# Optimization experiments

Hardware: AMD Instinct MI355X
Metric: run time of the kernel (lower is better)

## Reference

```python
import jax, jax.numpy as jnp
import numpy as np

EMBED_DIM = 1024
NUM_HEADS = 16
DEPTH = 12
HEAD_DIM = EMBED_DIM // NUM_HEADS // 2  # 32
LAMBDA_INIT = float(0.8 - 0.6 * np.exp(-0.3 * DEPTH))
B, T = 2, 2048


def setup_inputs() -> dict:
    key = jax.random.key(0)
    ks = jax.random.split(key, 10)
    s = 0.02
    return {
        "query": jax.random.normal(ks[0], (B, T, EMBED_DIM), jnp.float32),
        "Wq": jax.random.normal(ks[1], (EMBED_DIM, EMBED_DIM), jnp.float32) * s,
        "Wk": jax.random.normal(ks[2], (EMBED_DIM, EMBED_DIM), jnp.float32) * s,
        "Wv": jax.random.normal(ks[3], (EMBED_DIM, EMBED_DIM), jnp.float32) * s,
        "Wo": jax.random.normal(ks[4], (EMBED_DIM, EMBED_DIM), jnp.float32) * s,
        "lambda_q1": jax.random.normal(ks[5], (HEAD_DIM,), jnp.float32) * 0.1,
        "lambda_k1": jax.random.normal(ks[6], (HEAD_DIM,), jnp.float32) * 0.1,
        "lambda_q2": jax.random.normal(ks[7], (HEAD_DIM,), jnp.float32) * 0.1,
        "lambda_k2": jax.random.normal(ks[8], (HEAD_DIM,), jnp.float32) * 0.1,
        "subln_w": jnp.ones((2 * HEAD_DIM,), jnp.float32),
    }


def reference(query, Wq, Wk, Wv, Wo, lambda_q1, lambda_k1, lambda_q2, lambda_k2, subln_w):
    Bsz, Tt, E = query.shape
    H, hd = NUM_HEADS, HEAD_DIM
    scaling = hd ** -0.5
    # projections (torch Linear: x @ W.T), W stored [out, in]
    q = jnp.einsum('bte,fe->btf', query, Wq).reshape(Bsz, Tt, 2 * H, hd).transpose(0, 2, 1, 3)
    k = jnp.einsum('bse,fe->bsf', query, Wk).reshape(Bsz, Tt, 2 * H, hd).transpose(0, 2, 1, 3)
    v = jnp.einsum('bse,fe->bsf', query, Wv).reshape(Bsz, Tt, H, 2 * hd).transpose(0, 2, 1, 3)
    q = q * scaling
    # dual attention map [B, 2H, T, T], softmax in fp32
    scores = jnp.einsum('bhtd,bhsd->bhts', q, k)
    attn_w = jax.nn.softmax(scores.astype(jnp.float32), axis=-1).astype(q.dtype)
    # learned lambda
    lam1 = jnp.exp(jnp.sum(lambda_q1 * lambda_k1))
    lam2 = jnp.exp(jnp.sum(lambda_q2 * lambda_k2))
    lam = lam1 - lam2 + LAMBDA_INIT
    aw = attn_w.reshape(Bsz, H, 2, Tt, Tt)
    aw = aw[:, :, 0] - lam * aw[:, :, 1]  # [B, H, T, T]
    attn = jnp.einsum('bhts,bhsd->bhtd', aw, v)  # [B, H, T, 2*hd]
    # RMSNorm over last dim (fp32), eps=1e-5, elementwise affine
    x32 = attn.astype(jnp.float32)
    normed = (x32 * jax.lax.rsqrt(jnp.mean(x32 * x32, axis=-1, keepdims=True) + 1e-5)).astype(attn.dtype)
    attn = normed * subln_w
    attn = attn * (1.0 - LAMBDA_INIT)
    out = attn.transpose(0, 2, 1, 3).reshape(Bsz, Tt, H * 2 * hd)
    return jnp.einsum('bte,fe->btf', out, Wo)
```

## Files before the change

### kernel.cpp

```cpp
#include <hip/hip_runtime.h>

typedef short bf16x8 __attribute__((ext_vector_type(8)));
typedef float f32x4 __attribute__((ext_vector_type(4)));
typedef float f32x16 __attribute__((ext_vector_type(16)));
typedef unsigned short ushort_t;
typedef unsigned int uint32;

#define LAMBDA_INIT 0.7836057665316245f
#define TT 2048
#define EE 1024

__device__ __forceinline__ ushort_t f2bf(float x) {
  uint32 b = __float_as_uint(x);
  b += 0x7fffu + ((b >> 16) & 1u);
  return (ushort_t)(b >> 16);
}

__device__ __forceinline__ uint32 cvtpk(float lo, float hi) {
  uint32 r;
  asm("v_cvt_pk_bf16_f32 %0, %1, %2" : "=v"(r) : "v"(lo), "v"(hi));
  return r;
}

__device__ __forceinline__ float fexp2(float x) {
#if __has_builtin(__builtin_amdgcn_exp2f)
  return __builtin_amdgcn_exp2f(x);
#else
  return exp2f(x);
#endif
}

__device__ __forceinline__ bf16x8 mkfrag(uint32 a, uint32 b, uint32 c, uint32 d) {
  union { uint32 w[4]; bf16x8 v; } u;
  u.w[0] = a; u.w[1] = b; u.w[2] = c; u.w[3] = d;
  return u.v;
}

__device__ __forceinline__ void gload16(const void* g, void* l) {
  __builtin_amdgcn_global_load_lds(
      (const __attribute__((address_space(1))) uint32*)g,
      (__attribute__((address_space(3))) uint32*)l, 16, 0, 0);
}

__global__ __launch_bounds__(256) void cvt_all(const float* __restrict__ X,
                                               const float* __restrict__ Wq,
                                               const float* __restrict__ Wk,
                                               const float* __restrict__ Wv,
                                               const float* __restrict__ Wo,
                                               ushort_t* __restrict__ out) {
  const int i = blockIdx.x * 256 + threadIdx.x;
  const float* src;
  int off;
  if (i < 1048576)      { src = X;  off = 0; }
  else if (i < 1310720) { src = Wq; off = 1048576; }
  else if (i < 1572864) { src = Wk; off = 1310720; }
  else if (i < 1835008) { src = Wv; off = 1572864; }
  else                  { src = Wo; off = 1835008; }
  const float4 v = reinterpret_cast<const float4*>(src)[i - off];
  ushort4 o;
  o.x = f2bf(v.x); o.y = f2bf(v.y); o.z = f2bf(v.z); o.w = f2bf(v.w);
  reinterpret_cast<ushort4*>(out)[i] = o;
}

__global__ __launch_bounds__(256) void gemm_bt(const ushort_t* __restrict__ A,
                                               const ushort_t* __restrict__ B,
                                               float* __restrict__ C,
                                               int M, int N, int K, float scale) {
  __shared__ ushort_t As[128 * 32];
  __shared__ ushort_t Bs[128 * 32];
  const int tid = threadIdx.x;
  const int lane = tid & 63, wid = tid >> 6;
  const int wr = wid >> 1, wc = wid & 1;
  const int r16 = lane & 15, g = lane >> 4;
  const int m0 = blockIdx.x * 128, n0 = blockIdx.y * 128;
  f32x4 acc[4][4] = {};
  for (int k0 = 0; k0 < K; k0 += 32) {
#pragma unroll
    for (int c = 0; c < 2; ++c) {
      int eo = wid * 1024 + c * 512 + lane * 8;
      int row = eo >> 5, col = eo & 31;
      gload16(A + (size_t)(m0 + row) * K + k0 + col, As + wid * 1024 + c * 512);
      gload16(B + (size_t)(n0 + row) * K + k0 + col, Bs + wid * 1024 + c * 512);
    }
    __syncthreads();
    bf16x8 af[4], bfg[4];
#pragma unroll
    for (int m = 0; m < 4; ++m)
      af[m] = *reinterpret_cast<const bf16x8*>(As + (wr * 64 + m * 16 + r16) * 32 + g * 8);
#pragma unroll
    for (int n = 0; n < 4; ++n)
      bfg[n] = *reinterpret_cast<const bf16x8*>(Bs + (wc * 64 + n * 16 + r16) * 32 + g * 8);
#pragma unroll
    for (int m = 0; m < 4; ++m)
#pragma unroll
      for (int n = 0; n < 4; ++n)
        acc[m][n] = __builtin_amdgcn_mfma_f32_16x16x32_bf16(af[m], bfg[n], acc[m][n], 0, 0, 0);
    __syncthreads();
  }
#pragma unroll
  for (int m = 0; m < 4; ++m)
#pragma unroll
    for (int n = 0; n < 4; ++n)
#pragma unroll
      for (int r = 0; r < 4; ++r) {
        int row = m0 + wr * 64 + m * 16 + g * 4 + r;
        int col = n0 + wc * 64 + n * 16 + r16;
        C[(size_t)row * N + col] = acc[m][n][r] * scale;
      }
}

#define SHALF(Sbase, Gbase)                                                  \
  do {                                                                       \
    _Pragma("unroll") for (int j_ = 0; j_ < 2; ++j_) {                       \
      const int c_ = wid * 2 + j_;                                           \
      gload16((Gbase) + (size_t)(c_ * 8 + (lane >> 3)) * EE +                \
                  (((lane & 7) ^ (lane >> 3)) << 3),                         \
              (Sbase) + c_ * 512);                                           \
    }                                                                        \
  } while (0)

#define CHUNK(mp)                                                            \
  do {                                                                       \
    __builtin_amdgcn_s_setprio(1);                                           \
    _Pragma("unroll") for (int mm_ = 0; mm_ < 2; ++mm_) {                    \
      const int m_ = (mp) * 2 + mm_;                                         \
      _Pragma("unroll") for (int n_ = 0; n_ < 4; ++n_) {                     \
        acc[m_][n_] = __builtin_amdgcn_mfma_f32_16x16x32_bf16(               \
            af[m_][0], bfr[n_][0], acc[m_][n_], 0, 0, 0);                    \
        acc[m_][n_] = __builtin_amdgcn_mfma_f32_16x16x32_bf16(               \
            af[m_][1], bfr[n_][1], acc[m_][n_], 0, 0, 0);                    \
      }                                                                      \
    }                                                                        \
    __builtin_amdgcn_s_setprio(0);                                           \
  } while (0)

__global__ __launch_bounds__(512, 2) void qkv_gemm256(const ushort_t* __restrict__ A,
                                                      const ushort_t* __restrict__ B,
                                                      ushort_t* __restrict__ C,
                                                      float scale) {
  __shared__ ushort_t Asm[2][16384];
  __shared__ ushort_t Bsm[2][16384];
  const int NKT = EE / 64;
  const int tid = threadIdx.x, lane = tid & 63, wid = tid >> 6;
  const int wr = wid >> 2, wc = wid & 3;
  const int r16 = lane & 15, g = lane >> 4;
  const int w = (blockIdx.x & 7) * 24 + (blockIdx.x >> 3);
  const int bx = w & 15, by = w >> 4;
  const int m0 = bx * 256, n0 = by * 256;
  const ushort_t* Ab = A + (size_t)m0 * EE;
  const ushort_t* Bb = B + (size_t)n0 * EE;

#pragma unroll
  for (int kt = 0; kt < 2; ++kt) {
    SHALF(Asm[kt], Ab + kt * 64);
    SHALF(Asm[kt] + 8192, Ab + (size_t)128 * EE + kt * 64);
    SHALF(Bsm[kt], Bb + kt * 64);
    SHALF(Bsm[kt] + 8192, Bb + (size_t)128 * EE + kt * 64);
  }

  f32x4 acc[8][4] = {};
  for (int t = 0; t < NKT; ++t) {
    const int b = t & 1;
    if (t < NKT - 1) asm volatile("s_waitcnt vmcnt(8)" ::: "memory");
    else             asm volatile("s_waitcnt vmcnt(0)" ::: "memory");
    __builtin_amdgcn_s_barrier();
    asm volatile("" ::: "memory");
    bf16x8 af[8][2], bfr[4][2];
#pragma unroll
    for (int m = 0; m < 8; ++m) {
      const int row = wr * 128 + m * 16 + r16;
#pragma unroll
      for (int kk = 0; kk < 2; ++kk)
        af[m][kk] = *reinterpret_cast<const bf16x8*>(
            Asm[b] + row * 64 + (((kk * 4 + g) ^ (r16 & 7)) << 3));
    }
#pragma unroll
    for (int n = 0; n < 4; ++n) {
      const int row = wc * 64 + n * 16 + r16;
#pragma unroll
      for (int kk = 0; kk < 2; ++kk)
        bfr[n][kk] = *reinterpret_cast<const bf16x8*>(
            Bsm[b] + row * 64 + (((kk * 4 + g) ^ (r16 & 7)) << 3));
    }
    asm volatile("s_waitcnt lgkmcnt(0)" ::: "memory");
    __builtin_amdgcn_s_barrier();
    asm volatile("" ::: "memory");
    const int ts = t + 2;
    const bool st = ts < NKT;
    if (st) SHALF(Asm[b], Ab + ts * 64);
    CHUNK(0);
    if (st) SHALF(Asm[b] + 8192, Ab + (size_t)128 * EE + ts * 64);
    CHUNK(1);
    if (st) SHALF(Bsm[b], Bb + ts * 64);
    CHUNK(2);
    if (st) SHALF(Bsm[b] + 8192, Bb + (size_t)128 * EE + ts * 64);
    CHUNK(3);
  }

  const size_t MN = (size_t)4096 * EE;
#pragma unroll
  for (int m = 0; m < 8; ++m)
#pragma unroll
    for (int n = 0; n < 4; ++n) {
      const int col = n0 + wc * 64 + n * 16 + r16;
      const int seg = col >> 10;
      const int cl = col & 1023;
      if (seg == 2) {
        int row0 = m0 + wr * 128 + m * 16 + g * 4;
        int bb2 = row0 >> 11, t0v = row0 & (TT - 1);
        ushort4 pk;
        pk.x = f2bf(acc[m][n][0]); pk.y = f2bf(acc[m][n][1]);
        pk.z = f2bf(acc[m][n][2]); pk.w = f2bf(acc[m][n][3]);
        *reinterpret_cast<ushort4*>(
            C + 2 * MN + ((size_t)(bb2 * 16 + (cl >> 6)) * 64 + (cl & 63)) * TT + t0v) = pk;
      } else {
        const float sc = (seg == 0) ? scale : 1.0f;
        const size_t base = (size_t)seg * MN;
#pragma unroll
        for (int r = 0; r < 4; ++r) {
          int row = m0 + wr * 128 + m * 16 + g * 4 + r;
          C[base + (size_t)row * EE + cl] = f2bf(acc[m][n][r] * sc);
        }
      }
    }
}


#define PHALF(sv, lacc, oT0, oT1, vf)                                                   \
  do {                                                                                  \
    float p_[16];                                                                       \
    _Pragma("unroll") for (int i_ = 0; i_ < 16; ++i_) p_[i_] = fexp2(sv[i_]);           \
    lacc += (((p_[0] + p_[1]) + (p_[2] + p_[3])) + ((p_[4] + p_[5]) + (p_[6] + p_[7]))) \
          + (((p_[8] + p_[9]) + (p_[10] + p_[11])) +                                    \
             ((p_[12] + p_[13]) + (p_[14] + p_[15])));                                  \
    auto wA_ = __builtin_amdgcn_permlane32_swap((int)cvtpk(p_[0], p_[1]),               \
                                                (int)cvtpk(p_[4], p_[5]), false, false);\
    auto wB_ = __builtin_amdgcn_permlane32_swap((int)cvtpk(p_[2], p_[3]),               \
                                                (int)cvtpk(p_[6], p_[7]), false, false);\
    auto wC_ = __builtin_amdgcn_permlane32_swap((int)cvtpk(p_[8], p_[9]),               \
                                                (int)cvtpk(p_[12], p_[13]), false, false);\
    auto wD_ = __builtin_amdgcn_permlane32_swap((int)cvtpk(p_[10], p_[11]),             \
                                                (int)cvtpk(p_[14], p_[15]), false, false);\
    bf16x8 pa0_ = mkfrag(wA_[0], wB_[0], wA_[1], wB_[1]);                               \
    bf16x8 pa1_ = mkfrag(wC_[0], wD_[0], wC_[1], wD_[1]);                               \
    oT0 = __builtin_amdgcn_mfma_f32_32x32x16_bf16(pa0_, vf[0][0], oT0, 0, 0, 0);        \
    oT0 = __builtin_amdgcn_mfma_f32_32x32x16_bf16(pa1_, vf[1][0], oT0, 0, 0, 0);        \
    oT1 = __builtin_amdgcn_mfma_f32_32x32x16_bf16(pa0_, vf[0][1], oT1, 0, 0, 0);        \
    oT1 = __builtin_amdgcn_mfma_f32_32x32x16_bf16(pa1_, vf[1][1], oT1, 0, 0, 0);        \
  } while (0)

#define STAGE3(Kdst, Vdst, kv0)                                                         \
  do {                                                                                  \
    const int r8_ = lane >> 3;                                                          \
    const int g_ = (lane & 7) ^ r8_;                                                    \
    _Pragma("unroll") for (int c2_ = 0; c2_ < 2; ++c2_) {                               \
      const int c_ = wid * 2 + c2_;                                                     \
      gload16(Kg + (size_t)((kv0) + c_ * 8 + r8_) * EE + g_ * 8,                        \
              (Kdst) + c_ * 512);                                                       \
      gload16(Vg + (size_t)(c_ * 8 + r8_) * TT + (kv0) + g_ * 8,                        \
              (Vdst) + c_ * 512);                                                       \
    }                                                                                   \
  } while (0)

__global__ __launch_bounds__(256, 2) void attn_fused(
    const ushort_t* __restrict__ Q, const ushort_t* __restrict__ K,
    const ushort_t* __restrict__ Vt,
    const float* __restrict__ lq1, const float* __restrict__ lk1,
    const float* __restrict__ lq2, const float* __restrict__ lk2,
    const float* __restrict__ w, ushort_t* __restrict__ X2) {
  __shared__ ushort_t Ksm[3][64 * 64];
  __shared__ ushort_t Vsm[3][64 * 64];
  const int tid = threadIdx.x, lane = tid & 63, wid = tid >> 6;
  const int l31 = lane & 31, hh = lane >> 5;
  const int bid = blockIdx.x;
  const int slice = (bid & 7) + 8 * (bid >> 7);
  const int qb = (bid >> 3) & 15;
  const int bb = slice >> 4, h = slice & 15;
  const int q0 = qb * 128 + wid * 32;

  float prod = (lane < 32) ? lq1[l31] * lk1[l31] : lq2[l31] * lk2[l31];
#pragma unroll
  for (int off = 1; off < 32; off <<= 1) prod += __shfl_xor(prod, off, 32);
  const float lam = __expf(__shfl(prod, 0, 64)) - __expf(__shfl(prod, 32, 64)) + LAMBDA_INIT;

  const ushort_t* Qp = Q + (size_t)(bb * TT + q0 + l31) * EE + h * 64 + hh * 8;
  const bf16x8 qf00 = *reinterpret_cast<const bf16x8*>(Qp);
  const bf16x8 qf01 = *reinterpret_cast<const bf16x8*>(Qp + 16);
  const bf16x8 qf10 = *reinterpret_cast<const bf16x8*>(Qp + 32);
  const bf16x8 qf11 = *reinterpret_cast<const bf16x8*>(Qp + 48);

  const ushort_t* Kg = K + (size_t)bb * TT * EE + h * 64;
  const ushort_t* Vg = Vt + (size_t)(bb * 16 + h) * 64 * TT;
  const int swz = (l31 & 7) << 3;

  f32x16 o00 = {}, o01 = {}, o10 = {}, o11 = {};
  float l0 = 0.f, l1 = 0.f;

  STAGE3(Ksm[0], Vsm[0], 0);
  STAGE3(Ksm[1], Vsm[1], 64);
  for (int it = 0; it < 32; ++it) {
    const ushort_t* Kt_ = Ksm[it % 3];
    const ushort_t* Vt_ = Vsm[it % 3];
    if (it < 31) asm volatile("s_waitcnt vmcnt(4)" ::: "memory");
    else         asm volatile("s_waitcnt vmcnt(0)" ::: "memory");
    __builtin_amdgcn_s_barrier();
    asm volatile("" ::: "memory");
    if (it + 2 < 32) {
      const int nb = (it + 2) % 3;
      STAGE3(Ksm[nb], Vsm[nb], (it + 2) * 64);
    }
#pragma unroll
    for (int s = 0; s < 2; ++s) {
      bf16x8 kf[2][2], vf[2][2];
#pragma unroll
      for (int hf = 0; hf < 2; ++hf)
#pragma unroll
        for (int ks = 0; ks < 2; ++ks)
          kf[hf][ks] = *reinterpret_cast<const bf16x8*>(
              Kt_ + (s * 32 + l31) * 64 + ((hf * 32 + ks * 16 + hh * 8) ^ swz));
#pragma unroll
      for (int ks = 0; ks < 2; ++ks)
#pragma unroll
        for (int dc = 0; dc < 2; ++dc)
          vf[ks][dc] = *reinterpret_cast<const bf16x8*>(
              Vt_ + (dc * 32 + l31) * 64 + ((s * 32 + ks * 16 + hh * 8) ^ swz));

      __builtin_amdgcn_s_setprio(1);
      const f32x16 zz = {};
      f32x16 s0_ = __builtin_amdgcn_mfma_f32_32x32x16_bf16(kf[0][0], qf00, zz, 0, 0, 0);
      s0_ = __builtin_amdgcn_mfma_f32_32x32x16_bf16(kf[0][1], qf01, s0_, 0, 0, 0);
      f32x16 s1_ = __builtin_amdgcn_mfma_f32_32x32x16_bf16(kf[1][0], qf10, zz, 0, 0, 0);
      s1_ = __builtin_amdgcn_mfma_f32_32x32x16_bf16(kf[1][1], qf11, s1_, 0, 0, 0);
      __builtin_amdgcn_s_setprio(0);
      PHALF(s0_, l0, o00, o01, vf);
      PHALF(s1_, l1, o10, o11, vf);
    }
  }

  {
    auto t0 = __builtin_amdgcn_permlane32_swap(__float_as_int(l0), __float_as_int(l0),
                                               false, false);
    l0 = __int_as_float(t0[0]) + __int_as_float(t0[1]);
    auto t1 = __builtin_amdgcn_permlane32_swap(__float_as_int(l1), __float_as_int(l1),
                                               false, false);
    l1 = __int_as_float(t1[0]) + __int_as_float(t1[1]);
  }

  const float w0v = w[l31];
  const float w1v = w[32 + l31];
#pragma unroll
  for (int r = 0; r < 16; ++r) {
    const int qrel = (r & 3) + 8 * (r >> 2) + 4 * hh;
    const float il0 = 1.0f / __shfl(l0, qrel, 64);
    const float il1 = lam / __shfl(l1, qrel, 64);
    const float x0 = o00[r] * il0 - o10[r] * il1;
    const float x1 = o01[r] * il0 - o11[r] * il1;
    float ss = x0 * x0 + x1 * x1;
#pragma unroll
    for (int off = 1; off < 32; off <<= 1) ss += __shfl_xor(ss, off, 64);
    const float sc = rsqrtf(ss * (1.0f / 64.0f) + 1e-5f) * (1.0f - LAMBDA_INIT);
    const size_t ob = (size_t)(bb * TT + q0 + qrel) * EE + h * 64 + l31;
    X2[ob] = f2bf(x0 * sc * w0v);
    X2[ob + 32] = f2bf(x1 * sc * w1v);
  }
}

extern "C" void kernel_launch(void* const* d_in, const int* in_sizes, int n_in,
                              void* d_out, int out_size, void* d_ws, size_t ws_size,
                              hipStream_t stream) {
  const float* X = (const float*)d_in[0];
  const float* Wq = (const float*)d_in[1];
  const float* Wk = (const float*)d_in[2];
  const float* Wv = (const float*)d_in[3];
  const float* Wo = (const float*)d_in[4];
  const float* lq1 = (const float*)d_in[5];
  const float* lk1 = (const float*)d_in[6];
  const float* lq2 = (const float*)d_in[7];
  const float* lk2 = (const float*)d_in[8];
  const float* slw = (const float*)d_in[9];

  const int M = 4096, E = EE;

  ushort_t* Xb = (ushort_t*)d_ws;
  ushort_t* Wqb = Xb + (size_t)M * E;
  ushort_t* Wob = Wqb + (size_t)3 * E * E;
  ushort_t* Qb = Wob + (size_t)E * E;
  ushort_t* Kb = Qb + (size_t)M * E;
  ushort_t* Vtb = Kb + (size_t)M * E;
  ushort_t* X2 = Vtb + (size_t)M * E;

  cvt_all<<<8192, 256, 0, stream>>>(X, Wq, Wk, Wv, Wo, Xb);

  qkv_gemm256<<<192, 512, 0, stream>>>(Xb, Wqb, Qb,
                                       0.17677669529663687f * 1.4426950408889634f);

  attn_fused<<<512, 256, 0, stream>>>(Qb, Kb, Vtb, lq1, lk1, lq2, lk2, slw, X2);

  gemm_bt<<<dim3(M / 128, E / 128), 256, 0, stream>>>(X2, Wob, (float*)d_out, M, E, E,
                                                      1.0f);
}
```

Measured before the change: 136.8 us.

## Replace output projection GEMM with double-buffered, swizzled, pipelined kernel

The output projection GEMM moves from a single-buffered K=32 loop with two syncthreads per step to a K=64 tile, double-buffered LDS pipeline. Async global-to-LDS loads for step t+2 are issued while MFMAs run on step t. It also adds an XOR swizzle of LDS columns to avoid bank conflicts and a remapped block index for L2 locality. This targets load-latency stalls and barrier overhead, at the cost of more LDS use and reliance on hand-placed waitcnt counts.

```diff
diff --git a/kernel.cpp b/kernel.cpp
--- a/kernel.cpp
+++ b/kernel.cpp
@@ -62,50 +62,95 @@
   reinterpret_cast<ushort4*>(out)[i] = o;
 }
 
-__global__ __launch_bounds__(256) void gemm_bt(const ushort_t* __restrict__ A,
-                                               const ushort_t* __restrict__ B,
-                                               float* __restrict__ C,
-                                               int M, int N, int K, float scale) {
-  __shared__ ushort_t As[128 * 32];
-  __shared__ ushort_t Bs[128 * 32];
-  const int tid = threadIdx.x;
-  const int lane = tid & 63, wid = tid >> 6;
+#define OSHALF(Sbase, Gbase)                                                 \
+  do {                                                                       \
+    _Pragma("unroll") for (int j_ = 0; j_ < 4; ++j_) {                       \
+      const int c_ = wid * 4 + j_;                                           \
+      gload16((Gbase) + (size_t)(c_ * 8 + (lane >> 3)) * EE +                \
+                  (((lane & 7) ^ (lane >> 3)) << 3),                         \
+              (Sbase) + c_ * 512);                                           \
+    }                                                                        \
+  } while (0)
+
+#define OCHUNK(mp)                                                           \
+  do {                                                                       \
+    __builtin_amdgcn_s_setprio(1);                                           \
+    _Pragma("unroll") for (int n_ = 0; n_ < 4; ++n_) {                       \
+      acc[mp][n_] = __builtin_amdgcn_mfma_f32_16x16x32_bf16(                 \
+          af[mp][0], bfg[n_][0], acc[mp][n_], 0, 0, 0);                      \
+      acc[mp][n_] = __builtin_amdgcn_mfma_f32_16x16x32_bf16(                 \
+          af[mp][1], bfg[n_][1], acc[mp][n_], 0, 0, 0);                      \
+    }                                                                        \
+    __builtin_amdgcn_s_setprio(0);                                           \
+  } while (0)
+
+__global__ __launch_bounds__(256, 2) void outp_gemm(const ushort_t* __restrict__ A,
+                                                    const ushort_t* __restrict__ B,
+                                                    float* __restrict__ C) {
+  __shared__ ushort_t Asm[2][8192];
+  __shared__ ushort_t Bsm[2][8192];
+  const int NKT = EE / 64;
+  const int tid = threadIdx.x, lane = tid & 63, wid = tid >> 6;
   const int wr = wid >> 1, wc = wid & 1;
   const int r16 = lane & 15, g = lane >> 4;
-  const int m0 = blockIdx.x * 128, n0 = blockIdx.y * 128;
+  const int w = (blockIdx.x & 7) * 32 + (blockIdx.x >> 3);
+  const int bx = w & 31, by = w >> 5;
+  const int m0 = bx * 128, n0 = by * 128;
+  const ushort_t* Ab = A + (size_t)m0 * EE;
+  const ushort_t* Bb = B + (size_t)n0 * EE;
+
+#pragma unroll
+  for (int kt = 0; kt < 2; ++kt) {
+    OSHALF(Asm[kt], Ab + kt * 64);
+    OSHALF(Bsm[kt], Bb + kt * 64);
+  }
+
   f32x4 acc[4][4] = {};
-  for (int k0 = 0; k0 < K; k0 += 32) {
-#pragma unroll
-    for (int c = 0; c < 2; ++c) {
-      int eo = wid * 1024 + c * 512 + lane * 8;
-      int row = eo >> 5, col = eo & 31;
-      gload16(A + (size_t)(m0 + row) * K + k0 + col, As + wid * 1024 + c * 512);
-      gload16(B + (size_t)(n0 + row) * K + k0 + col, Bs + wid * 1024 + c * 512);
-    }
-    __syncthreads();
-    bf16x8 af[4], bfg[4];
-#pragma unroll
-    for (int m = 0; m < 4; ++m)
-      af[m] = *reinterpret_cast<const bf16x8*>(As + (wr * 64 + m * 16 + r16) * 32 + g * 8);
+  for (int t = 0; t < NKT; ++t) {
+    const int b = t & 1;
+    if (t < NKT - 1) asm volatile("s_waitcnt vmcnt(8)" ::: "memory");
+    else             asm volatile("s_waitcnt vmcnt(0)" ::: "memory");
+    __builtin_amdgcn_s_barrier();
+    asm volatile("" ::: "memory");
+    bf16x8 af[4][2], bfg[4][2];
+#pragma unroll
+    for (int m = 0; m < 4; ++m) {
+      const int row = wr * 64 + m * 16 + r16;
+#pragma unroll
+      for (int kk = 0; kk < 2; ++kk)
+        af[m][kk] = *reinterpret_cast<const bf16x8*>(
+            Asm[b] + row * 64 + (((kk * 4 + g) ^ (r16 & 7)) << 3));
+    }
+#pragma unroll
+    for (int n = 0; n < 4; ++n) {
+      const int row = wc * 64 + n * 16 + r16;
+#pragma unroll
+      for (int kk = 0; kk < 2; ++kk)
+        bfg[n][kk] = *reinterpret_cast<const bf16x8*>(
+            Bsm[b] + row * 64 + (((kk * 4 + g) ^ (r16 & 7)) << 3));
+    }
+    asm volatile("s_waitcnt lgkmcnt(0)" ::: "memory");
+    __builtin_amdgcn_s_barrier();
+    asm volatile("" ::: "memory");
+    const int ts = t + 2;
+    const bool st = ts < NKT;
+    if (st) OSHALF(Asm[b], Ab + ts * 64);
+    OCHUNK(0);
+    OCHUNK(1);
+    if (st) OSHALF(Bsm[b], Bb + ts * 64);
+    OCHUNK(2);
+    OCHUNK(3);
+  }
+
+#pragma unroll
+  for (int m = 0; m < 4; ++m)
 #pragma unroll
     for (int n = 0; n < 4; ++n)
-      bfg[n] = *reinterpret_cast<const bf16x8*>(Bs + (wc * 64 + n * 16 + r16) * 32 + g * 8);
-#pragma unroll
-    for (int m = 0; m < 4; ++m)
-#pragma unroll
-      for (int n = 0; n < 4; ++n)
-        acc[m][n] = __builtin_amdgcn_mfma_f32_16x16x32_bf16(af[m], bfg[n], acc[m][n], 0, 0, 0);
-    __syncthreads();
-  }
-#pragma unroll
-  for (int m = 0; m < 4; ++m)
-#pragma unroll
-    for (int n = 0; n < 4; ++n)
 #pragma unroll
       for (int r = 0; r < 4; ++r) {
-        int row = m0 + wr * 64 + m * 16 + g * 4 + r;
-        int col = n0 + wc * 64 + n * 16 + r16;
-        C[(size_t)row * N + col] = acc[m][n][r] * scale;
+        const int row = m0 + wr * 64 + m * 16 + g * 4 + r;
+        const int col = n0 + wc * 64 + n * 16 + r16;
+        C[(size_t)row * EE + col] = acc[m][n][r];
       }
 }
 
@@ -224,7 +269,6 @@
       }
     }
 }
-
 
 #define PHALF(sv, lacc, oT0, oT1, vf)                                                   \
   do {                                                                                  \
@@ -396,6 +440,5 @@
 
   attn_fused<<<512, 256, 0, stream>>>(Qb, Kb, Vtb, lq1, lk1, lq2, lk2, slw, X2);
 
-  gemm_bt<<<dim3(M / 128, E / 128), 256, 0, stream>>>(X2, Wob, (float*)d_out, M, E, E,
-                                                      1.0f);
-}
+  outp_gemm<<<256, 256, 0, stream>>>(X2, Wob, (float*)d_out);
+}
```

New measurement: 131.8 us, median of 2. -3.6%, faster.
